# Kernel optimization log

Hardware: AMD Instinct MI355X
Metric: run time of the kernel (lower is better)

## Reference

```python
import jax, jax.numpy as jnp
import numpy as np
from jax import lax

B, T, H, L = 1024, 512, 64, 3


def setup_inputs() -> dict:
    key = jax.random.key(0)
    ks = jax.random.split(key, 7)
    s = 1.0 / np.sqrt(H)  # pytorch default init scale (uniform bound); randn*s is fine for a numeric reference
    return {
        "x": jax.random.normal(ks[0], (B, T, H), dtype=jnp.float32),
        "W_ih": jax.random.normal(ks[1], (L, H, H), dtype=jnp.float32) * s,
        "W_hh": jax.random.normal(ks[2], (L, H, H), dtype=jnp.float32) * s,
        "b_ih": jax.random.normal(ks[3], (L, H), dtype=jnp.float32) * s,
        "b_hh": jax.random.normal(ks[4], (L, H), dtype=jnp.float32) * s,
        "fc_w": jax.random.normal(ks[5], (1, H), dtype=jnp.float32) * s,
        "fc_b": jax.random.normal(ks[6], (1,), dtype=jnp.float32) * s,
    }


def _run_layer(x_seq, Wih, Whh, bih, bhh):
    # x_seq: [B, T, Hin]; precompute the input projection once (parallel over T)
    xproj = jnp.einsum("bti,hi->bth", x_seq, Wih) + bih  # [B, T, H]

    def step(h, xt):
        h = jnp.tanh(xt + h @ Whh.T + bhh)
        return h, h

    h0 = jnp.zeros((x_seq.shape[0], Whh.shape[0]), dtype=x_seq.dtype)
    _, ys = lax.scan(step, h0, jnp.swapaxes(xproj, 0, 1))  # scan over time
    return jnp.swapaxes(ys, 0, 1)  # [B, T, H]


def reference(x, W_ih, W_hh, b_ih, b_hh, fc_w, fc_b):
    h = x
    for l in range(L):  # small fixed layer count
        h = _run_layer(h, W_ih[l], W_hh[l], b_ih[l], b_hh[l])
    # fc applied to last timestep only
    return h[:, -1, :] @ fc_w.T + fc_b  # [B, 1]
```

## Files before the change

### kernel.cpp

```cpp
#include <hip/hip_runtime.h>


typedef __attribute__((ext_vector_type(2))) float f32x2;
typedef __attribute__((ext_vector_type(4))) float f32x4;

#define RNN_B 1024
#define RNN_T 512
#define RNN_H 64
#define WPB   4

static __device__ __forceinline__ f32x2 mk2(float a, float b) {
    f32x2 r; r.x = a; r.y = b; return r;
}

__global__ __launch_bounds__(256, 1)
void rnn_layer_fused(const float* __restrict__ in,
                     float*       __restrict__ out,
                     const float* __restrict__ Wih,
                     const float* __restrict__ Whh,
                     const float* __restrict__ bih,
                     const float* __restrict__ bhh,
                     const float* __restrict__ fcw,
                     const float* __restrict__ fcb,
                     float*       __restrict__ fcout,
                     int is_last)
{
    __shared__ f32x4 lds[WPB][2][RNN_H / 4];

    const int lane = threadIdx.x & 63;
    const int wid  = threadIdx.x >> 6;
    const int b    = blockIdx.x * WPB + wid;

    f32x2 wih2[RNN_H / 2], whh2[RNN_H / 2];
    {
        const f32x4* wr = (const f32x4*)(Wih + (size_t)lane * RNN_H);
        const f32x4* hr = (const f32x4*)(Whh + (size_t)lane * RNN_H);
#pragma unroll
        for (int c = 0; c < RNN_H / 4; ++c) {
            f32x4 a = wr[c];
            wih2[2*c+0] = mk2(a.x, a.y);
            wih2[2*c+1] = mk2(a.z, a.w);
            f32x4 d = hr[c];
            whh2[2*c+0] = mk2(d.x, d.y);
            whh2[2*c+1] = mk2(d.z, d.w);
        }
    }
#pragma unroll
    for (int i = 0; i < RNN_H / 2; ++i)
        asm volatile("" : "+v"(wih2[i]), "+v"(whh2[i]));

    const float bias = bih[lane] + bhh[lane];

    float* xl = (float*)&lds[wid][0][0];
    float* hl = (float*)&lds[wid][1][0];

    const float* inrow  = in + (size_t)b * RNN_T * RNN_H;
    float*       outrow = is_last ? nullptr : out + (size_t)b * RNN_T * RNN_H;

    xl[lane] = inrow[lane];
    hl[lane] = 0.0f;
    float xreg = inrow[RNN_H + lane];
    float hval = 0.0f;

    for (int t = 0; t < RNN_T; ++t) {
        f32x4 xv[RNN_H / 4], hv[RNN_H / 4];
#pragma unroll
        for (int c = 0; c < RNN_H / 4; ++c) xv[c] = lds[wid][0][c];
#pragma unroll
        for (int c = 0; c < RNN_H / 4; ++c) hv[c] = lds[wid][1][c];

        f32x2 a0 = mk2(0.f, 0.f), a1 = mk2(0.f, 0.f);
        f32x2 a2 = mk2(0.f, 0.f), a3 = mk2(0.f, 0.f);
#pragma unroll
        for (int c = 0; c < RNN_H / 4; ++c) {
            a0 += mk2(xv[c].x, xv[c].y) * wih2[2*c+0];
            a1 += mk2(xv[c].z, xv[c].w) * wih2[2*c+1];
            a2 += mk2(hv[c].x, hv[c].y) * whh2[2*c+0];
            a3 += mk2(hv[c].z, hv[c].w) * whh2[2*c+1];
        }
        const f32x2 s = (a0 + a1) + (a2 + a3);
        const float pre = (s.x + s.y) + bias;

        const float ax = fabsf(pre);
        const float e  = __expf(-2.0f * ax);
        const float r  = (1.0f - e) / (1.0f + e);
        hval = copysignf(r, pre);

        hl[lane] = hval;
        if (t + 1 < RNN_T) {
            xl[lane] = xreg;
            const int tn = (t + 2 < RNN_T) ? (t + 2) : (t + 1);
            xreg = inrow[(size_t)tn * RNN_H + lane];
        }
        if (!is_last) outrow[(size_t)t * RNN_H + lane] = hval;
    }

    if (is_last) {
        float p = hval * fcw[lane];
#pragma unroll
        for (int off = 32; off > 0; off >>= 1)
            p += __shfl_xor(p, off, 64);
        if (lane == 0) fcout[b] = p + fcb[0];
    }
}

extern "C" void kernel_launch(void* const* d_in, const int* in_sizes, int n_in,
                              void* d_out, int out_size, void* d_ws, size_t ws_size,
                              hipStream_t stream)
{
    const float* x   = (const float*)d_in[0];
    const float* Wih = (const float*)d_in[1];
    const float* Whh = (const float*)d_in[2];
    const float* bih = (const float*)d_in[3];
    const float* bhh = (const float*)d_in[4];
    const float* fcw = (const float*)d_in[5];
    const float* fcb = (const float*)d_in[6];
    float* out  = (float*)d_out;
    float* hseq = (float*)d_ws;

    dim3 grid(RNN_B / WPB);
    dim3 block(WPB * 64);

    rnn_layer_fused<<<grid, block, 0, stream>>>(
        x, hseq, Wih, Whh, bih, bhh, nullptr, nullptr, nullptr, 0);
    rnn_layer_fused<<<grid, block, 0, stream>>>(
        hseq, hseq, Wih + RNN_H * RNN_H, Whh + RNN_H * RNN_H,
        bih + RNN_H, bhh + RNN_H, nullptr, nullptr, nullptr, 0);
    rnn_layer_fused<<<grid, block, 0, stream>>>(
        hseq, nullptr, Wih + 2 * RNN_H * RNN_H, Whh + 2 * RNN_H * RNN_H,
        bih + 2 * RNN_H, bhh + 2 * RNN_H, fcw, fcb, out, 1);
}
```

Before: 826.2 us.

## Fuse three RNN layers into one wavefront-pipelined kernel per batch row

```diff
diff --git a/kernel.cpp b/kernel.cpp
--- a/kernel.cpp
+++ b/kernel.cpp
@@ -7,100 +7,111 @@
 #define RNN_B 1024
 #define RNN_T 512
 #define RNN_H 64
-#define WPB   4
+#define RNN_L 3
 
 static __device__ __forceinline__ f32x2 mk2(float a, float b) {
     f32x2 r; r.x = a; r.y = b; return r;
 }
 
-__global__ __launch_bounds__(256, 1)
-void rnn_layer_fused(const float* __restrict__ in,
-                     float*       __restrict__ out,
-                     const float* __restrict__ Wih,
-                     const float* __restrict__ Whh,
-                     const float* __restrict__ bih,
-                     const float* __restrict__ bhh,
-                     const float* __restrict__ fcw,
-                     const float* __restrict__ fcb,
-                     float*       __restrict__ fcout,
-                     int is_last)
+__global__ __launch_bounds__(192, 3)
+void rnn_pipeline(const float* __restrict__ x,
+                  const float* __restrict__ Wih,
+                  const float* __restrict__ Whh,
+                  const float* __restrict__ bih,
+                  const float* __restrict__ bhh,
+                  const float* __restrict__ fcw,
+                  const float* __restrict__ fcb,
+                  float* __restrict__ out)
 {
-    __shared__ f32x4 lds[WPB][2][RNN_H / 4];
+    __shared__ f32x4 ring[RNN_L + 1][2][RNN_H / 4];
 
     const int lane = threadIdx.x & 63;
-    const int wid  = threadIdx.x >> 6;
-    const int b    = blockIdx.x * WPB + wid;
+    const int l    = threadIdx.x >> 6;
+    const int b    = blockIdx.x;
 
-    f32x2 wih2[RNN_H / 2], whh2[RNN_H / 2];
+    f32x2 wi[RNN_H / 2], wh[RNN_H / 2];
     {
-        const f32x4* wr = (const f32x4*)(Wih + (size_t)lane * RNN_H);
-        const f32x4* hr = (const f32x4*)(Whh + (size_t)lane * RNN_H);
+        const f32x4* wr = (const f32x4*)(Wih + ((size_t)l * RNN_H + lane) * RNN_H);
+        const f32x4* hr = (const f32x4*)(Whh + ((size_t)l * RNN_H + lane) * RNN_H);
 #pragma unroll
         for (int c = 0; c < RNN_H / 4; ++c) {
             f32x4 a = wr[c];
-            wih2[2*c+0] = mk2(a.x, a.y);
-            wih2[2*c+1] = mk2(a.z, a.w);
+            wi[2*c+0] = mk2(a.x, a.y); wi[2*c+1] = mk2(a.z, a.w);
             f32x4 d = hr[c];
-            whh2[2*c+0] = mk2(d.x, d.y);
-            whh2[2*c+1] = mk2(d.z, d.w);
+            wh[2*c+0] = mk2(d.x, d.y); wh[2*c+1] = mk2(d.z, d.w);
         }
     }
 #pragma unroll
     for (int i = 0; i < RNN_H / 2; ++i)
-        asm volatile("" : "+v"(wih2[i]), "+v"(whh2[i]));
+        asm volatile("" : "+v"(wi[i]), "+v"(wh[i]));
 
-    const float bias = bih[lane] + bhh[lane];
+    const float bias = bih[l * RNN_H + lane] + bhh[l * RNN_H + lane];
+    const float fw   = fcw[lane];
+    const float fb   = fcb[0];
 
-    float* xl = (float*)&lds[wid][0][0];
-    float* hl = (float*)&lds[wid][1][0];
+    ((float*)&ring[l][0][0])[lane] = 0.0f;
+    ((float*)&ring[l][1][0])[lane] = 0.0f;
 
-    const float* inrow  = in + (size_t)b * RNN_T * RNN_H;
-    float*       outrow = is_last ? nullptr : out + (size_t)b * RNN_T * RNN_H;
+    const float* xrow = x + (size_t)b * RNN_T * RNN_H;
+    float xr = 0.0f, xn = 0.0f;
+    if (l == 0) {
+        ((float*)&ring[3][0][0])[lane] = xrow[lane];
+        xr = xrow[RNN_H + lane];
+        xn = xrow[2 * RNN_H + lane];
+    }
+    __syncthreads();
 
-    xl[lane] = inrow[lane];
-    hl[lane] = 0.0f;
-    float xreg = inrow[RNN_H + lane];
+    const int in_ring = (l == 0) ? 3 : (l - 1);
     float hval = 0.0f;
 
-    for (int t = 0; t < RNN_T; ++t) {
-        f32x4 xv[RNN_H / 4], hv[RNN_H / 4];
+    for (int s = 0; s < RNN_T + RNN_L - 1; ++s) {
+        const int t = s - l;
+        const bool active = (t >= 0) && (t < RNN_T);
+        if (active) {
+            const int si = t & 1;
+            const int sh = (t - 1) & 1;
+
+            f32x2 a0 = mk2(bias, 0.0f), a1 = mk2(0.f, 0.f);
+            f32x2 a2 = mk2(0.f, 0.f),   a3 = mk2(0.f, 0.f);
 #pragma unroll
-        for (int c = 0; c < RNN_H / 4; ++c) xv[c] = lds[wid][0][c];
+            for (int c = 0; c < RNN_H / 4; ++c) {
+                f32x4 v = ring[in_ring][si][c];
+                a0 += mk2(v.x, v.y) * wi[2*c+0];
+                a1 += mk2(v.z, v.w) * wi[2*c+1];
+            }
 #pragma unroll
-        for (int c = 0; c < RNN_H / 4; ++c) hv[c] = lds[wid][1][c];
+            for (int c = 0; c < RNN_H / 4; ++c) {
+                f32x4 v = ring[l][sh][c];
+                a2 += mk2(v.x, v.y) * wh[2*c+0];
+                a3 += mk2(v.z, v.w) * wh[2*c+1];
+            }
+            const f32x2 ss = (a0 + a2) + (a1 + a3);
+            const float pre = ss.x + ss.y;
 
-        f32x2 a0 = mk2(0.f, 0.f), a1 = mk2(0.f, 0.f);
-        f32x2 a2 = mk2(0.f, 0.f), a3 = mk2(0.f, 0.f);
+            const float ax = fabsf(pre);
+            const float e  = __expf(-2.0f * ax);
+            const float r  = (1.0f - e) / (1.0f + e);
+            hval = copysignf(r, pre);
+
+            ((float*)&ring[l][t & 1][0])[lane] = hval;
+
+            if (l == 0) {
+                if (t + 1 < RNN_T)
+                    ((float*)&ring[3][(t + 1) & 1][0])[lane] = xr;
+                xr = xn;
+                const int tn = (t + 3 < RNN_T) ? (t + 3) : (RNN_T - 1);
+                xn = xrow[(size_t)tn * RNN_H + lane];
+            }
+
+            if (l == 2 && t == RNN_T - 1) {
+                float p = hval * fw;
 #pragma unroll
-        for (int c = 0; c < RNN_H / 4; ++c) {
-            a0 += mk2(xv[c].x, xv[c].y) * wih2[2*c+0];
-            a1 += mk2(xv[c].z, xv[c].w) * wih2[2*c+1];
-            a2 += mk2(hv[c].x, hv[c].y) * whh2[2*c+0];
-            a3 += mk2(hv[c].z, hv[c].w) * whh2[2*c+1];
+                for (int off = 32; off > 0; off >>= 1)
+                    p += __shfl_xor(p, off, 64);
+                if (lane == 0) out[b] = p + fb;
+            }
         }
-        const f32x2 s = (a0 + a1) + (a2 + a3);
-        const float pre = (s.x + s.y) + bias;
-
-        const float ax = fabsf(pre);
-        const float e  = __expf(-2.0f * ax);
-        const float r  = (1.0f - e) / (1.0f + e);
-        hval = copysignf(r, pre);
-
-        hl[lane] = hval;
-        if (t + 1 < RNN_T) {
-            xl[lane] = xreg;
-            const int tn = (t + 2 < RNN_T) ? (t + 2) : (t + 1);
-            xreg = inrow[(size_t)tn * RNN_H + lane];
-        }
-        if (!is_last) outrow[(size_t)t * RNN_H + lane] = hval;
-    }
-
-    if (is_last) {
-        float p = hval * fcw[lane];
-#pragma unroll
-        for (int off = 32; off > 0; off >>= 1)
-            p += __shfl_xor(p, off, 64);
-        if (lane == 0) fcout[b] = p + fcb[0];
+        __syncthreads();
     }
 }
 
@@ -115,18 +126,8 @@
     const float* bhh = (const float*)d_in[4];
     const float* fcw = (const float*)d_in[5];
     const float* fcb = (const float*)d_in[6];
-    float* out  = (float*)d_out;
-    float* hseq = (float*)d_ws;
+    float* out = (float*)d_out;
 
-    dim3 grid(RNN_B / WPB);
-    dim3 block(WPB * 64);
-
-    rnn_layer_fused<<<grid, block, 0, stream>>>(
-        x, hseq, Wih, Whh, bih, bhh, nullptr, nullptr, nullptr, 0);
-    rnn_layer_fused<<<grid, block, 0, stream>>>(
-        hseq, hseq, Wih + RNN_H * RNN_H, Whh + RNN_H * RNN_H,
-        bih + RNN_H, bhh + RNN_H, nullptr, nullptr, nullptr, 0);
-    rnn_layer_fused<<<grid, block, 0, stream>>>(
-        hseq, nullptr, Wih + 2 * RNN_H * RNN_H, Whh + 2 * RNN_H * RNN_H,
-        bih + 2 * RNN_H, bhh + 2 * RNN_H, fcw, fcb, out, 1);
+    rnn_pipeline<<<dim3(RNN_B), dim3(RNN_L * 64), 0, stream>>>(
+        x, Wih, Whh, bih, bhh, fcw, fcb, out);
 }
```

Result: slower. 1.131 ms (median of 2 runs) (+36.8%).
